# Kernel tuning notes

Hardware: AMD Instinct MI355X
Metric: run time of the kernel (lower is better)

Reference implementation:

```python
import jax, jax.numpy as jnp
import numpy as np

N_NODES = 50000
N_EDGES = 800000
D = 512
N_LAYERS = 3
LN_EPS = 1e-5


def _layer_norm(h, gamma, beta):
    mu = jnp.mean(h, axis=-1, keepdims=True)
    var = jnp.mean(jnp.square(h - mu), axis=-1, keepdims=True)
    return (h - mu) * jax.lax.rsqrt(var + LN_EPS) * gamma + beta


def setup_inputs() -> dict:
    key = jax.random.key(0)
    ks = jax.random.split(key, 5)
    x = jax.random.normal(ks[0], (N_NODES, D), dtype=jnp.float32)
    edge_index = jax.random.randint(ks[1], (2, N_EDGES), 0, N_NODES, dtype=jnp.int64)
    edge_weight = jax.random.uniform(ks[2], (N_EDGES,), dtype=jnp.float32)
    # GCNConv lin weights (xavier-ish scale), zero biases; LayerNorm affine params
    Ws = jax.random.normal(ks[3], (N_LAYERS, D, D), dtype=jnp.float32) * (1.0 / np.sqrt(D))
    bs = jnp.zeros((N_LAYERS, D), dtype=jnp.float32)
    gammas = jnp.ones((N_LAYERS, D), dtype=jnp.float32)
    betas = jnp.zeros((N_LAYERS, D), dtype=jnp.float32)
    return {"x": x, "edge_index": edge_index, "edge_weight": edge_weight,
            "Ws": Ws, "bs": bs, "gammas": gammas, "betas": betas}


def reference(x, edge_index, edge_weight, Ws, bs, gammas, betas):
    n = x.shape[0]
    row, col = edge_index[0], edge_index[1]  # source -> target (PyG convention)
    # add self loops with weight 1 (GCNConv add_self_loops=True)
    sl = jnp.arange(n, dtype=edge_index.dtype)
    row2 = jnp.concatenate([row, sl])
    col2 = jnp.concatenate([col, sl])
    ew = jnp.concatenate([edge_weight, jnp.ones((n,), dtype=edge_weight.dtype)])
    # symmetric normalization: D^{-1/2} A D^{-1/2}
    deg = jax.ops.segment_sum(ew, col2, num_segments=n)
    dinv = jnp.where(deg > 0, 1.0 / jnp.sqrt(jnp.where(deg > 0, deg, 1.0)), 0.0)
    norm = dinv[row2] * ew * dinv[col2]  # [E+N]

    for i in range(N_LAYERS):
        identity = x
        h = x @ Ws[i].T                       # [N, D] linear transform
        msg = norm[:, None] * h[row2]         # gather + scale per edge
        agg = jax.ops.segment_sum(msg, col2, num_segments=n) + bs[i]
        h = _layer_norm(agg, gammas[i], betas[i])
        if i < N_LAYERS - 1:
            h = jax.nn.relu(h)                # dropout=0 -> identity
        x = h + identity                      # residual (dims equal -> Identity proj)
    return x
```

## Files before the change

### kernel.cpp

```cpp
#include <hip/hip_runtime.h>
#include <hip/hip_bf16.h>
#include <stdint.h>

#define D 512
#define LN_EPS 1e-5f

typedef __attribute__((ext_vector_type(8))) short bf16x8;
typedef __attribute__((ext_vector_type(4))) float f32x4;

__device__ __forceinline__ unsigned short f32_to_bf16_bits(float x) {
    unsigned int u = __float_as_uint(x);
    u += 0x7fffu + ((u >> 16) & 1u);
    return (unsigned short)(u >> 16);
}
__device__ __forceinline__ float bf16lo(unsigned int u) { return __uint_as_float(u << 16); }
__device__ __forceinline__ float bf16hi(unsigned int u) { return __uint_as_float(u & 0xffff0000u); }

typedef const __attribute__((address_space(1))) unsigned int GU;
typedef __attribute__((address_space(3))) unsigned int LU;
__device__ __forceinline__ void gload_lds16(const void* g, void* l) {
    __builtin_amdgcn_global_load_lds((GU*)g, (LU*)l, 16, 0, 0);
}

__global__ void k_prep(const float4* __restrict__ x0, ushort4* __restrict__ xb4,
                       const float4* __restrict__ Ws4, ushort4* __restrict__ wb4,
                       float* __restrict__ deg, int* __restrict__ cnt,
                       long nx4, long nxin4, long nw4, int N) {
    long id = (long)blockIdx.x * blockDim.x + threadIdx.x;
    if (id < nx4) {
        float4 v;
        if (id < nxin4) v = x0[id];
        else { v.x = 0.f; v.y = 0.f; v.z = 0.f; v.w = 0.f; }
        ushort4 o;
        o.x = f32_to_bf16_bits(v.x);
        o.y = f32_to_bf16_bits(v.y);
        o.z = f32_to_bf16_bits(v.z);
        o.w = f32_to_bf16_bits(v.w);
        xb4[id] = o;
    } else if (id < nx4 + nw4) {
        long i = id - nx4;
        float4 v = Ws4[i];
        ushort4 o;
        o.x = f32_to_bf16_bits(v.x);
        o.y = f32_to_bf16_bits(v.y);
        o.z = f32_to_bf16_bits(v.z);
        o.w = f32_to_bf16_bits(v.w);
        wb4[i] = o;
    } else {
        long i = id - nx4 - nw4;
        if (i < N) { deg[i] = 1.0f; cnt[i] = 1; }
    }
}

__global__ void k_deg_cnt(const int* __restrict__ col, const float* __restrict__ ew,
                          float* deg, int* cnt, int E) {
    int e = blockIdx.x * blockDim.x + threadIdx.x;
    if (e < E) {
        int c = col[e];
        atomicAdd(&deg[c], ew[e]);
        atomicAdd(&cnt[c], 1);
    }
}

__global__ __launch_bounds__(1024) void k_scan(const int* __restrict__ cnt,
                                               float* __restrict__ deg,
                                               int* __restrict__ rptr,
                                               int* __restrict__ cur, int n) {
    for (int i = threadIdx.x; i < n; i += 1024) deg[i] = rsqrtf(deg[i]);

    const int tid = threadIdx.x, lane = tid & 63, wv = tid >> 6;
    const int chunk = (n + 15) >> 4;
    const int wbeg = wv * chunk;
    const int wend = min(wbeg + chunk, n);

    int tot = 0;
    for (int i = wbeg + lane; i < wend; i += 64) tot += cnt[i];
#pragma unroll
    for (int off = 32; off > 0; off >>= 1) tot += __shfl_xor(tot, off);
    __shared__ int woff[17];
    if (lane == 0) woff[wv] = tot;
    __syncthreads();
    if (tid == 0) {
        int r = 0;
        for (int w = 0; w < 16; ++w) { int t = woff[w]; woff[w] = r; r += t; }
        woff[16] = r;
    }
    __syncthreads();

    int run = woff[wv];
    for (int base = wbeg; base < wend; base += 64) {
        int i = base + lane;
        int v = (i < wend) ? cnt[i] : 0;
        int inc = v;
#pragma unroll
        for (int off = 1; off < 64; off <<= 1) {
            int u = __shfl_up(inc, off);
            if (lane >= off) inc += u;
        }
        if (i < wend) {
            int excl = run + inc - v;
            rptr[i] = excl;
            cur[i] = excl;
        }
        run += __shfl(inc, 63);
    }
    if (tid == 0) rptr[n] = woff[16];
}

__global__ void k_fill(const int* __restrict__ row, const int* __restrict__ col,
                       const float* __restrict__ ew, const float* __restrict__ dinv,
                       int* cur, uint2* __restrict__ srcval, int N, int E) {
    int i = blockIdx.x * blockDim.x + threadIdx.x;
    if (i < N) {
        int slot = atomicAdd(&cur[i], 1);
        float d = dinv[i];
        uint2 sv; sv.x = (unsigned)i; sv.y = __float_as_uint(d * d);
        srcval[slot] = sv;
    } else if (i < N + E) {
        int e = i - N;
        int r = row[e], c = col[e];
        int slot = atomicAdd(&cur[c], 1);
        uint2 sv; sv.x = (unsigned)r;
        sv.y = __float_as_uint(dinv[r] * ew[e] * dinv[c]);
        srcval[slot] = sv;
    }
}

__global__ __launch_bounds__(512) void k_gemm(
    const short* __restrict__ A,
    const short* __restrict__ W,
    short* __restrict__ H,
    int Mpad) {
    __shared__ short As[64 * 32];
    __shared__ short Bs[512 * 32];
    const int tid = threadIdx.x;
    const int wave = tid >> 6, lane = tid & 63;
    const int wn = wave * 64;
    const int tm = blockIdx.x * 64;
    f32x4 acc[4][4] = {};
    const int fr = lane & 15, fc = lane >> 4;

    const int r0 = tid >> 2, cb0 = (tid & 3) * 8;
    const short* Ab = A + (size_t)(tm + r0) * 512 + cb0;
    const short* Wb = W + (size_t)r0 * 512 + cb0;

    for (int k0 = 0; k0 < 512; k0 += 32) {
        if (tid < 256) gload_lds16(Ab + k0, &As[tid * 8]);
        gload_lds16(Wb + k0,                     &Bs[tid * 8]);
        gload_lds16(Wb + (size_t)128 * 512 + k0, &Bs[(tid + 512) * 8]);
        gload_lds16(Wb + (size_t)256 * 512 + k0, &Bs[(tid + 1024) * 8]);
        gload_lds16(Wb + (size_t)384 * 512 + k0, &Bs[(tid + 1536) * 8]);
        __syncthreads();
        bf16x8 af[4], bfr[4];
#pragma unroll
        for (int m = 0; m < 4; ++m)
            af[m] = *(const bf16x8*)&As[(m * 16 + fr) * 32 + fc * 8];
#pragma unroll
        for (int n = 0; n < 4; ++n)
            bfr[n] = *(const bf16x8*)&Bs[(wn + n * 16 + fr) * 32 + fc * 8];
#pragma unroll
        for (int m = 0; m < 4; ++m) {
#pragma unroll
            for (int n = 0; n < 4; ++n)
                acc[m][n] = __builtin_amdgcn_mfma_f32_16x16x32_bf16(af[m], bfr[n], acc[m][n], 0, 0, 0);
        }
        __syncthreads();
    }
    const int cbase = wn + (lane & 15);
    const int rbase = tm + fc * 4;
#pragma unroll
    for (int m = 0; m < 4; ++m) {
#pragma unroll
        for (int n = 0; n < 4; ++n) {
#pragma unroll
            for (int j = 0; j < 4; ++j) {
                int r = rbase + m * 16 + j;
                int c = cbase + n * 16;
                H[(size_t)r * 512 + c] = (short)f32_to_bf16_bits(acc[m][n][j]);
            }
        }
    }
}

__global__ __launch_bounds__(256) void k_agg_ln(
    const uint4* __restrict__ H4,
    const int* __restrict__ rptr,
    const uint2* __restrict__ srcval,
    const float4* __restrict__ bias,
    const float4* __restrict__ gamma,
    const float4* __restrict__ beta,
    uint4* __restrict__ xb,
    float4* __restrict__ out_f32,
    int N, int last) {
    const int wv = threadIdx.x >> 6, lane = threadIdx.x & 63;
    const int t = blockIdx.x * 4 + wv;
    if (t >= N) return;
    const int beg = rptr[t], end = rptr[t + 1];

    float a[8], b[8];
#pragma unroll
    for (int i = 0; i < 8; ++i) { a[i] = 0.f; b[i] = 0.f; }

    for (int base = beg; base < end; base += 64) {
        int m = end - base;
        if (m > 64) m = 64;
        int idx = base + lane;
        if (idx > end - 1) idx = end - 1;
        uint2 svl = srcval[idx];
        int e = 0;
        for (; e + 2 <= m; e += 2) {
            unsigned s0 = __shfl(svl.x, e);
            unsigned s1 = __shfl(svl.x, e + 1);
            float w0 = __uint_as_float(__shfl(svl.y, e));
            float w1 = __uint_as_float(__shfl(svl.y, e + 1));
            uint4 u0 = H4[(size_t)s0 * 64 + lane];
            uint4 u1 = H4[(size_t)s1 * 64 + lane];
            a[0] = fmaf(w0, bf16lo(u0.x), a[0]);
            a[1] = fmaf(w0, bf16hi(u0.x), a[1]);
            a[2] = fmaf(w0, bf16lo(u0.y), a[2]);
            a[3] = fmaf(w0, bf16hi(u0.y), a[3]);
            a[4] = fmaf(w0, bf16lo(u0.z), a[4]);
            a[5] = fmaf(w0, bf16hi(u0.z), a[5]);
            a[6] = fmaf(w0, bf16lo(u0.w), a[6]);
            a[7] = fmaf(w0, bf16hi(u0.w), a[7]);
            b[0] = fmaf(w1, bf16lo(u1.x), b[0]);
            b[1] = fmaf(w1, bf16hi(u1.x), b[1]);
            b[2] = fmaf(w1, bf16lo(u1.y), b[2]);
            b[3] = fmaf(w1, bf16hi(u1.y), b[3]);
            b[4] = fmaf(w1, bf16lo(u1.z), b[4]);
            b[5] = fmaf(w1, bf16hi(u1.z), b[5]);
            b[6] = fmaf(w1, bf16lo(u1.w), b[6]);
            b[7] = fmaf(w1, bf16hi(u1.w), b[7]);
        }
        if (e < m) {
            unsigned s0 = __shfl(svl.x, e);
            float w0 = __uint_as_float(__shfl(svl.y, e));
            uint4 u0 = H4[(size_t)s0 * 64 + lane];
            a[0] = fmaf(w0, bf16lo(u0.x), a[0]);
            a[1] = fmaf(w0, bf16hi(u0.x), a[1]);
            a[2] = fmaf(w0, bf16lo(u0.y), a[2]);
            a[3] = fmaf(w0, bf16hi(u0.y), a[3]);
            a[4] = fmaf(w0, bf16lo(u0.z), a[4]);
            a[5] = fmaf(w0, bf16hi(u0.z), a[5]);
            a[6] = fmaf(w0, bf16lo(u0.w), a[6]);
            a[7] = fmaf(w0, bf16hi(u0.w), a[7]);
        }
    }
#pragma unroll
    for (int i = 0; i < 8; ++i) a[i] += b[i];

    float4 bv0 = bias[lane * 2], bv1 = bias[lane * 2 + 1];
    a[0] += bv0.x; a[1] += bv0.y; a[2] += bv0.z; a[3] += bv0.w;
    a[4] += bv1.x; a[5] += bv1.y; a[6] += bv1.z; a[7] += bv1.w;

    float s1 = 0.f, s2 = 0.f;
#pragma unroll
    for (int i = 0; i < 8; ++i) { s1 += a[i]; s2 += a[i] * a[i]; }
#pragma unroll
    for (int off = 32; off > 0; off >>= 1) {
        s1 += __shfl_xor(s1, off);
        s2 += __shfl_xor(s2, off);
    }
    const float mean = s1 * (1.0f / 512.0f);
    const float var = s2 * (1.0f / 512.0f) - mean * mean;
    const float rstd = rsqrtf(var + LN_EPS);

    float4 gv0 = gamma[lane * 2], gv1 = gamma[lane * 2 + 1];
    float4 bt0 = beta[lane * 2], bt1 = beta[lane * 2 + 1];
    float o[8];
    o[0] = (a[0] - mean) * rstd * gv0.x + bt0.x;
    o[1] = (a[1] - mean) * rstd * gv0.y + bt0.y;
    o[2] = (a[2] - mean) * rstd * gv0.z + bt0.z;
    o[3] = (a[3] - mean) * rstd * gv0.w + bt0.w;
    o[4] = (a[4] - mean) * rstd * gv1.x + bt1.x;
    o[5] = (a[5] - mean) * rstd * gv1.y + bt1.y;
    o[6] = (a[6] - mean) * rstd * gv1.z + bt1.z;
    o[7] = (a[7] - mean) * rstd * gv1.w + bt1.w;
    if (!last) {
#pragma unroll
        for (int i = 0; i < 8; ++i) o[i] = fmaxf(o[i], 0.f);
    }
    uint4 idu = xb[(size_t)t * 64 + lane];
    o[0] += bf16lo(idu.x); o[1] += bf16hi(idu.x);
    o[2] += bf16lo(idu.y); o[3] += bf16hi(idu.y);
    o[4] += bf16lo(idu.z); o[5] += bf16hi(idu.z);
    o[6] += bf16lo(idu.w); o[7] += bf16hi(idu.w);

    if (last) {
        float4 f0, f1;
        f0.x = o[0]; f0.y = o[1]; f0.z = o[2]; f0.w = o[3];
        f1.x = o[4]; f1.y = o[5]; f1.z = o[6]; f1.w = o[7];
        out_f32[(size_t)t * 128 + lane * 2] = f0;
        out_f32[(size_t)t * 128 + lane * 2 + 1] = f1;
    } else {
        uint4 pk;
        pk.x = ((unsigned)f32_to_bf16_bits(o[1]) << 16) | f32_to_bf16_bits(o[0]);
        pk.y = ((unsigned)f32_to_bf16_bits(o[3]) << 16) | f32_to_bf16_bits(o[2]);
        pk.z = ((unsigned)f32_to_bf16_bits(o[5]) << 16) | f32_to_bf16_bits(o[4]);
        pk.w = ((unsigned)f32_to_bf16_bits(o[7]) << 16) | f32_to_bf16_bits(o[6]);
        xb[(size_t)t * 64 + lane] = pk;
    }
}

extern "C" void kernel_launch(void* const* d_in, const int* in_sizes, int n_in,
                              void* d_out, int out_size, void* d_ws, size_t ws_size,
                              hipStream_t stream) {
    const float* x0     = (const float*)d_in[0];
    const int*   ei     = (const int*)d_in[1];
    const float* ew     = (const float*)d_in[2];
    const float* Ws     = (const float*)d_in[3];
    const float* bs     = (const float*)d_in[4];
    const float* gammas = (const float*)d_in[5];
    const float* betas  = (const float*)d_in[6];

    const int N = in_sizes[0] / D;
    const int E = in_sizes[1] / 2;
    const int L = in_sizes[3] / (D * D);
    const int Mpad = (N + 63) & ~63;

    char* p = (char*)d_ws;
    auto carve = [&](size_t bytes) {
        char* q = p;
        p += (bytes + 255) & ~(size_t)255;
        return (void*)q;
    };
    short* xb     = (short*)carve((size_t)Mpad * D * 2);
    short* hb     = (short*)carve((size_t)Mpad * D * 2);
    short* wb     = (short*)carve((size_t)L * D * D * 2);
    float* dinv   = (float*)carve((size_t)N * 4);
    int*   cnt    = (int*)carve((size_t)N * 4);
    int*   rptr   = (int*)carve((size_t)(N + 1) * 4);
    int*   cur    = (int*)carve((size_t)N * 4);
    uint2* srcval = (uint2*)carve((size_t)(E + N) * 8);
    (void)ws_size; (void)n_in; (void)out_size;

    const int* rowI = ei;
    const int* colI = ei + E;

    {
        long nx4 = (long)Mpad * D / 4, nxin4 = (long)N * D / 4;
        long nw4 = (long)L * D * D / 4;
        long tot = nx4 + nw4 + N;
        k_prep<<<(int)((tot + 255) / 256), 256, 0, stream>>>(
            (const float4*)x0, (ushort4*)xb, (const float4*)Ws, (ushort4*)wb,
            dinv, cnt, nx4, nxin4, nw4, N);
    }
    k_deg_cnt<<<(E + 255) / 256, 256, 0, stream>>>(colI, ew, dinv, cnt, E);
    k_scan<<<1, 1024, 0, stream>>>(cnt, dinv, rptr, cur, N);
    k_fill<<<(N + E + 255) / 256, 256, 0, stream>>>(rowI, colI, ew, dinv, cur, srcval, N, E);

    for (int l = 0; l < L; ++l) {
        k_gemm<<<Mpad / 64, 512, 0, stream>>>(xb, wb + (size_t)l * D * D, hb, Mpad);
        int last = (l == L - 1);
        k_agg_ln<<<(N + 3) / 4, 256, 0, stream>>>(
            (const uint4*)hb, rptr, srcval,
            (const float4*)(bs + (size_t)l * D),
            (const float4*)(gammas + (size_t)l * D),
            (const float4*)(betas + (size_t)l * D),
            (uint4*)xb, (float4*)d_out, N, last);
    }
}
```

Baseline: 727.2 us.

## Retile GEMM to 128x256 blocks with double-buffered LDS prefetch

The GEMM kernel changes from 64x512 output tiles per block to 128x256 tiles on a 2D grid, with 8 waves arranged 2x4. The A and W k-slices are now double-buffered in LDS, so the next slice is prefetched while MFMAs run on the current one. This removes one barrier per k-step and is meant to hide global load latency while balancing A and W reuse. Mpad is rounded to a multiple of 128 to fit the new M tile, which adds a few padded rows.

Measured after the change: 700.2 us. 3.7% less time.

```diff
diff --git a/kernel.cpp b/kernel.cpp
--- a/kernel.cpp
+++ b/kernel.cpp
@@ -131,33 +131,39 @@
     const short* __restrict__ W,
     short* __restrict__ H,
     int Mpad) {
-    __shared__ short As[64 * 32];
-    __shared__ short Bs[512 * 32];
+    __shared__ short As[2][128 * 32];
+    __shared__ short Bs[2][256 * 32];
     const int tid = threadIdx.x;
     const int wave = tid >> 6, lane = tid & 63;
-    const int wn = wave * 64;
-    const int tm = blockIdx.x * 64;
+    const int wm = (wave >> 2) * 64, wn = (wave & 3) * 64;
+    const int tm = blockIdx.x * 128, tn = blockIdx.y * 256;
     f32x4 acc[4][4] = {};
     const int fr = lane & 15, fc = lane >> 4;
 
     const int r0 = tid >> 2, cb0 = (tid & 3) * 8;
     const short* Ab = A + (size_t)(tm + r0) * 512 + cb0;
-    const short* Wb = W + (size_t)r0 * 512 + cb0;
-
+    const short* Wb = W + (size_t)(tn + r0) * 512 + cb0;
+
+    gload_lds16(Ab,                     &As[0][tid * 8]);
+    gload_lds16(Wb,                     &Bs[0][tid * 8]);
+    gload_lds16(Wb + (size_t)128 * 512, &Bs[0][(tid + 512) * 8]);
+    __syncthreads();
+
+    int cur = 0;
     for (int k0 = 0; k0 < 512; k0 += 32) {
-        if (tid < 256) gload_lds16(Ab + k0, &As[tid * 8]);
-        gload_lds16(Wb + k0,                     &Bs[tid * 8]);
-        gload_lds16(Wb + (size_t)128 * 512 + k0, &Bs[(tid + 512) * 8]);
-        gload_lds16(Wb + (size_t)256 * 512 + k0, &Bs[(tid + 1024) * 8]);
-        gload_lds16(Wb + (size_t)384 * 512 + k0, &Bs[(tid + 1536) * 8]);
-        __syncthreads();
+        const int kn = k0 + 32;
+        if (kn < 512) {
+            gload_lds16(Ab + kn,                     &As[cur ^ 1][tid * 8]);
+            gload_lds16(Wb + kn,                     &Bs[cur ^ 1][tid * 8]);
+            gload_lds16(Wb + (size_t)128 * 512 + kn, &Bs[cur ^ 1][(tid + 512) * 8]);
+        }
         bf16x8 af[4], bfr[4];
 #pragma unroll
         for (int m = 0; m < 4; ++m)
-            af[m] = *(const bf16x8*)&As[(m * 16 + fr) * 32 + fc * 8];
+            af[m] = *(const bf16x8*)&As[cur][(wm + m * 16 + fr) * 32 + fc * 8];
 #pragma unroll
         for (int n = 0; n < 4; ++n)
-            bfr[n] = *(const bf16x8*)&Bs[(wn + n * 16 + fr) * 32 + fc * 8];
+            bfr[n] = *(const bf16x8*)&Bs[cur][(wn + n * 16 + fr) * 32 + fc * 8];
 #pragma unroll
         for (int m = 0; m < 4; ++m) {
 #pragma unroll
@@ -165,9 +171,10 @@
                 acc[m][n] = __builtin_amdgcn_mfma_f32_16x16x32_bf16(af[m], bfr[n], acc[m][n], 0, 0, 0);
         }
         __syncthreads();
-    }
-    const int cbase = wn + (lane & 15);
-    const int rbase = tm + fc * 4;
+        cur ^= 1;
+    }
+    const int cbase = tn + wn + (lane & 15);
+    const int rbase = tm + wm + fc * 4;
 #pragma unroll
     for (int m = 0; m < 4; ++m) {
 #pragma unroll
@@ -316,7 +323,7 @@
     const int N = in_sizes[0] / D;
     const int E = in_sizes[1] / 2;
     const int L = in_sizes[3] / (D * D);
-    const int Mpad = (N + 63) & ~63;
+    const int Mpad = (N + 127) & ~127;
 
     char* p = (char*)d_ws;
     auto carve = [&](size_t bytes) {
@@ -350,7 +357,8 @@
     k_fill<<<(N + E + 255) / 256, 256, 0, stream>>>(rowI, colI, ew, dinv, cur, srcval, N, E);
 
     for (int l = 0; l < L; ++l) {
-        k_gemm<<<Mpad / 64, 512, 0, stream>>>(xb, wb + (size_t)l * D * D, hb, Mpad);
+        dim3 g(Mpad / 128, D / 256);
+        k_gemm<<<g, 512, 0, stream>>>(xb, wb + (size_t)l * D * D, hb, Mpad);
         int last = (l == L - 1);
         k_agg_ln<<<(N + 3) / 4, 256, 0, stream>>>(
             (const uint4*)hb, rptr, srcval,
```
